# Performance work log

Hardware: AMD Instinct MI355X
Metric: run time of the kernel (lower is better)

Reference implementation:

```python
import jax, jax.numpy as jnp
import numpy as np

N_EMBD = 2048
N_HEAD = 16
N_KV_HEAD = 4
HD = N_EMBD // N_HEAD  # 128
B, T = 1, 4096
EPS = 1e-6


def apply_rope(x, cos, sin):
    # x: [B,T,H,hd]; cos/sin: [T,1,hd//2]
    hd = x.shape[-1] // 2
    x1, x2 = x[..., :hd], x[..., hd:]
    y1 = x1 * cos + x2 * sin
    y2 = x2 * cos - x1 * sin
    return jnp.concatenate((y1, y2), axis=-1).astype(x.dtype)


def rms_norm(x, eps=EPS):
    return x * jax.lax.rsqrt(jnp.mean(jnp.square(x), axis=-1, keepdims=True) + eps)


def setup_inputs() -> dict:
    key = jax.random.key(0)
    ks = jax.random.split(key, 7)
    s = 0.02
    return {
        "x": jax.random.normal(ks[0], (B, T, N_EMBD), dtype=jnp.float32),
        "cos": jax.random.normal(ks[1], (T, 1, HD // 2), dtype=jnp.float32),
        "sin": jax.random.normal(ks[2], (T, 1, HD // 2), dtype=jnp.float32),
        "wq": jax.random.normal(ks[3], (N_EMBD, N_HEAD * HD), dtype=jnp.float32) * s,
        "wk": jax.random.normal(ks[4], (N_EMBD, N_KV_HEAD * HD), dtype=jnp.float32) * s,
        "wv": jax.random.normal(ks[5], (N_EMBD, N_KV_HEAD * HD), dtype=jnp.float32) * s,
        "wo": jax.random.normal(ks[6], (N_EMBD, N_EMBD), dtype=jnp.float32) * s,
    }


def reference(x, cos, sin, wq, wk, wv, wo):
    Bb, Tt, C = x.shape
    q = (x @ wq).reshape(Bb, Tt, N_HEAD, HD)
    k = (x @ wk).reshape(Bb, Tt, N_KV_HEAD, HD)
    v = (x @ wv).reshape(Bb, Tt, N_KV_HEAD, HD)
    q = rms_norm(apply_rope(q, cos, sin))
    k = rms_norm(apply_rope(k, cos, sin))
    g = N_HEAD // N_KV_HEAD
    if g > 1:
        k = jnp.repeat(k, g, axis=2)  # [B,T,H,hd]
        v = jnp.repeat(v, g, axis=2)
    scale = 1.0 / jnp.sqrt(jnp.float32(HD))
    # scores: [B,H,T,S]
    scores = jnp.einsum("bthd,bshd->bhts", q, k) * scale
    causal = jnp.tril(jnp.ones((Tt, Tt), dtype=bool))
    scores = jnp.where(causal, scores, jnp.finfo(scores.dtype).min)
    attn = jax.nn.softmax(scores, axis=-1)
    y = jnp.einsum("bhts,bshd->bthd", attn, v).reshape(Bb, Tt, C)
    return y @ wo
```

## Files before the change

kernel.cpp:

```cpp
#include <hip/hip_runtime.h>

#define T_SEQ 4096
#define C_EMB 2048
#define NH 16
#define NKV 4
#define HD 128

typedef short bf16x8 __attribute__((ext_vector_type(8)));
typedef float f32x4 __attribute__((ext_vector_type(4)));
typedef unsigned short u16x4 __attribute__((ext_vector_type(4)));

__device__ inline unsigned short f2bf(float f) {
    unsigned int u = __float_as_uint(f);
    unsigned int r = (u + 0x7FFFu + ((u >> 16) & 1u)) >> 16;
    return (unsigned short)r;
}

__device__ __forceinline__ void async_cp16(const unsigned short* g, unsigned short* l) {
    __builtin_amdgcn_global_load_lds((const __attribute__((address_space(1))) unsigned int*)g,
                                     (__attribute__((address_space(3))) unsigned int*)l,
                                     16, 0, 0);
}

__global__ __launch_bounds__(256) void cvt_bf16(const float* __restrict__ in,
                                                unsigned short* __restrict__ out, int n) {
    int i = (blockIdx.x * 256 + threadIdx.x) * 4;
    if (i >= n) return;
    float4 f = *(const float4*)(&in[i]);
    u16x4 o;
    o.x = f2bf(f.x); o.y = f2bf(f.y); o.z = f2bf(f.z); o.w = f2bf(f.w);
    *(u16x4*)(&out[i]) = o;
}

__global__ __launch_bounds__(256) void transpose_cvt(const float* __restrict__ in, int ld_in,
                                                     int R, int Cc,
                                                     unsigned short* __restrict__ out, int ld_out) {
    __shared__ float tile[32][33];
    int x = blockIdx.x * 32 + threadIdx.x;
    for (int i = threadIdx.y; i < 32; i += 8) {
        int y = blockIdx.y * 32 + i;
        tile[i][threadIdx.x] = in[(size_t)y * ld_in + x];
    }
    __syncthreads();
    int xo = blockIdx.y * 32 + threadIdx.x;
    for (int i = threadIdx.y; i < 32; i += 8) {
        int yo = blockIdx.x * 32 + i;
        out[(size_t)yo * ld_out + xo] = f2bf(tile[threadIdx.x][i]);
    }
}

__global__ __launch_bounds__(256) void gemm_bt(const unsigned short* __restrict__ A,
                                               const unsigned short* __restrict__ Bt,
                                               float* __restrict__ C, int M, int N, int K) {
    __shared__ __align__(16) unsigned short As[128 * 64];
    __shared__ __align__(16) unsigned short Bs[128 * 64];
    int t = threadIdx.x;
    int w = t >> 6, lane = t & 63;
    int ln = lane & 15, q = lane >> 4;
    int wm = (w >> 1) * 64, wn = (w & 1) * 64;
    int m0 = blockIdx.y * 128, n0 = blockIdx.x * 128;

    f32x4 acc[4][4] = {};

    for (int k0 = 0; k0 < K; k0 += 64) {
        __syncthreads();
#pragma unroll
        for (int s = 0; s < 4; ++s) {
            int L = s * 256 + t;
            int r = L >> 3;
            int c = (L & 7) ^ (r & 7);
            async_cp16(&A[(size_t)(m0 + r) * K + k0 + c * 8], &As[s * 2048 + w * 512]);
            async_cp16(&Bt[(size_t)(n0 + r) * K + k0 + c * 8], &Bs[s * 2048 + w * 512]);
        }
        __syncthreads();
#pragma unroll
        for (int ks = 0; ks < 2; ++ks) {
            int cs = ((ks * 4 + q) ^ (ln & 7)) * 8;
            bf16x8 af[4], bfr[4];
#pragma unroll
            for (int i = 0; i < 4; ++i) af[i] = *(const bf16x8*)(&As[(wm + i * 16 + ln) * 64 + cs]);
#pragma unroll
            for (int j = 0; j < 4; ++j) bfr[j] = *(const bf16x8*)(&Bs[(wn + j * 16 + ln) * 64 + cs]);
#pragma unroll
            for (int i = 0; i < 4; ++i)
#pragma unroll
                for (int j = 0; j < 4; ++j)
                    acc[i][j] = __builtin_amdgcn_mfma_f32_16x16x32_bf16(af[i], bfr[j], acc[i][j], 0, 0, 0);
        }
    }
#pragma unroll
    for (int i = 0; i < 4; ++i)
#pragma unroll
        for (int j = 0; j < 4; ++j)
#pragma unroll
            for (int r = 0; r < 4; ++r) {
                int row = m0 + wm + i * 16 + q * 4 + r;
                int col = n0 + wn + j * 16 + ln;
                C[(size_t)row * N + col] = acc[i][j][r];
            }
}

__global__ __launch_bounds__(256) void rope_rms(const float* __restrict__ QKV,
                                                const float* __restrict__ cosb,
                                                const float* __restrict__ sinb,
                                                unsigned short* __restrict__ Qn,
                                                unsigned short* __restrict__ Kn) {
    int gw = blockIdx.x * 4 + (threadIdx.x >> 6);
    int lane = threadIdx.x & 63;
    int t = gw / 20;
    int h = gw % 20;
    const float* v = QKV + (size_t)t * 3072 + h * 128;
    float a = v[lane];
    float b = v[lane + 64];
    float cc = cosb[t * 64 + lane];
    float ss = sinb[t * 64 + lane];
    float y1 = a * cc + b * ss;
    float y2 = b * cc - a * ss;
    float sq = y1 * y1 + y2 * y2;
#pragma unroll
    for (int off = 1; off < 64; off <<= 1) sq += __shfl_xor(sq, off);
    float r = rsqrtf(sq * (1.0f / 128.0f) + 1e-6f);
    if (h < 16) {
        float s = r * (0.08838834764831845f * 1.4426950408889634f);
        unsigned short* o = Qn + (size_t)t * 2048 + h * 128;
        o[lane] = f2bf(y1 * s);
        o[lane + 64] = f2bf(y2 * s);
    } else {
        unsigned short* o = Kn + (size_t)t * 512 + (h - 16) * 128;
        o[lane] = f2bf(y1 * r);
        o[lane + 64] = f2bf(y2 * r);
    }
}

__global__ __launch_bounds__(256) void flash_attn(const unsigned short* __restrict__ Qn,
                                                  const unsigned short* __restrict__ Kn,
                                                  const unsigned short* __restrict__ Vt,
                                                  unsigned short* __restrict__ Ao) {
    __shared__ __align__(16) unsigned short Ks[2][64 * 128];
    __shared__ __align__(16) unsigned short Vs[2][128 * 64];
    __shared__ __align__(16) unsigned short Pl[4][16 * 72];

    int pairi = blockIdx.x;
    int h = blockIdx.y;
    int kvh = h >> 2;
    int t = threadIdx.x;
    int w = t >> 6, lane = t & 63;
    int ln = lane & 15, q = lane >> 4;

    int nA = 64 - pairi;
    int bq = 63 - pairi;
    int wq0 = bq * 64 + w * 16;

    bf16x8 qf[4];
    {
        const unsigned short* qb = Qn + (size_t)(wq0 + ln) * 2048 + h * 128;
#pragma unroll
        for (int kc = 0; kc < 4; ++kc) qf[kc] = *(const bf16x8*)(qb + kc * 32 + q * 8);
    }

    f32x4 o[8] = {};
    f32x4 l_p = {0.f, 0.f, 0.f, 0.f};

#pragma unroll
    for (int s = 0; s < 4; ++s) {
        int L = s * 256 + t;
        int key = L >> 4;
        int c = (L & 15) ^ (key & 15);
        async_cp16(Kn + (size_t)key * 512 + kvh * 128 + c * 8, &Ks[0][s * 2048 + w * 512]);
    }
#pragma unroll
    for (int s = 0; s < 4; ++s) {
        int L = s * 256 + t;
        int hd = L >> 3;
        int c = (L & 7) ^ (hd & 7);
        async_cp16(Vt + (size_t)(kvh * 128 + hd) * 4096 + c * 8, &Vs[0][s * 2048 + w * 512]);
    }

    for (int it = 0; it < 65; ++it) {
        __syncthreads();

        int nxt = it + 1;
        if (nxt < 65) {
            int nkt = (nxt < nA) ? nxt * 64 : (nxt - nA) * 64;
            unsigned short* kd = Ks[nxt & 1];
            unsigned short* vd = Vs[nxt & 1];
#pragma unroll
            for (int s = 0; s < 4; ++s) {
                int L = s * 256 + t;
                int key = L >> 4;
                int c = (L & 15) ^ (key & 15);
                async_cp16(Kn + (size_t)(nkt + key) * 512 + kvh * 128 + c * 8,
                           kd + s * 2048 + w * 512);
            }
#pragma unroll
            for (int s = 0; s < 4; ++s) {
                int L = s * 256 + t;
                int hd = L >> 3;
                int c = (L & 7) ^ (hd & 7);
                async_cp16(Vt + (size_t)(kvh * 128 + hd) * 4096 + nkt + c * 8,
                           vd + s * 2048 + w * 512);
            }
        }

        if (it == nA) {
#pragma unroll
            for (int r = 0; r < 4; ++r) {
                float lsum = l_p[r];
                lsum += __shfl_xor(lsum, 1);
                lsum += __shfl_xor(lsum, 2);
                lsum += __shfl_xor(lsum, 4);
                lsum += __shfl_xor(lsum, 8);
                float inv = 1.0f / lsum;
                int row = wq0 + q * 4 + r;
                unsigned short* ob = Ao + (size_t)row * 2048 + h * 128;
#pragma unroll
                for (int f = 0; f < 8; ++f) ob[f * 16 + ln] = f2bf(o[f][r] * inv);
            }
            bq = pairi;
            wq0 = bq * 64 + w * 16;
            const unsigned short* qb = Qn + (size_t)(wq0 + ln) * 2048 + h * 128;
#pragma unroll
            for (int kc = 0; kc < 4; ++kc) qf[kc] = *(const bf16x8*)(qb + kc * 32 + q * 8);
#pragma unroll
            for (int f = 0; f < 8; ++f) o[f] = (f32x4){0.f, 0.f, 0.f, 0.f};
            l_p = (f32x4){0.f, 0.f, 0.f, 0.f};
        }

        int kt0 = (it < nA) ? it * 64 : (it - nA) * 64;
        const unsigned short* kb = Ks[it & 1];
        const unsigned short* vb = Vs[it & 1];

        f32x4 sA[4] = {{-16.6f, -16.6f, -16.6f, -16.6f}, {-16.6f, -16.6f, -16.6f, -16.6f},
                       {-16.6f, -16.6f, -16.6f, -16.6f}, {-16.6f, -16.6f, -16.6f, -16.6f}};
#pragma unroll
        for (int jt = 0; jt < 4; ++jt) {
            int key = jt * 16 + ln;
#pragma unroll
            for (int kc = 0; kc < 4; ++kc) {
                int cs = ((kc * 4 + q) ^ ln) * 8;
                bf16x8 kf = *(const bf16x8*)(&kb[key * 128 + cs]);
                sA[jt] = __builtin_amdgcn_mfma_f32_16x16x32_bf16(qf[kc], kf, sA[jt], 0, 0, 0);
            }
        }
        if (kt0 + 63 > wq0) {
#pragma unroll
            for (int jt = 0; jt < 4; ++jt)
#pragma unroll
                for (int r = 0; r < 4; ++r) {
                    int key = kt0 + jt * 16 + ln;
                    int row = wq0 + q * 4 + r;
                    if (key > row) sA[jt][r] = -3e38f;
                }
        }
#pragma unroll
        for (int r = 0; r < 4; ++r) {
            int prow = (q * 4 + r) * 72;
#pragma unroll
            for (int jt = 0; jt < 4; ++jt) {
                float p = __builtin_amdgcn_exp2f(sA[jt][r]);
                Pl[w][prow + jt * 16 + ln] = (unsigned short)(__float_as_uint(p) >> 16);
                l_p[r] += p;
            }
        }

#pragma unroll
        for (int ks = 0; ks < 2; ++ks) {
            bf16x8 pa = *(const bf16x8*)(&Pl[w][ln * 72 + ks * 32 + q * 8]);
            int cs = ((ks * 4 + q) ^ (ln & 7)) * 8;
#pragma unroll
            for (int f = 0; f < 8; ++f) {
                bf16x8 vf = *(const bf16x8*)(&vb[(f * 16 + ln) * 64 + cs]);
                o[f] = __builtin_amdgcn_mfma_f32_16x16x32_bf16(pa, vf, o[f], 0, 0, 0);
            }
        }
    }
#pragma unroll
    for (int r = 0; r < 4; ++r) {
        float lsum = l_p[r];
        lsum += __shfl_xor(lsum, 1);
        lsum += __shfl_xor(lsum, 2);
        lsum += __shfl_xor(lsum, 4);
        lsum += __shfl_xor(lsum, 8);
        float inv = 1.0f / lsum;
        int row = wq0 + q * 4 + r;
        unsigned short* ob = Ao + (size_t)row * 2048 + h * 128;
#pragma unroll
        for (int f = 0; f < 8; ++f) ob[f * 16 + ln] = f2bf(o[f][r] * inv);
    }
}

extern "C" void kernel_launch(void* const* d_in, const int* in_sizes, int n_in,
                              void* d_out, int out_size, void* d_ws, size_t ws_size,
                              hipStream_t stream) {
    const float* x    = (const float*)d_in[0];
    const float* cosb = (const float*)d_in[1];
    const float* sinb = (const float*)d_in[2];
    const float* wq   = (const float*)d_in[3];
    const float* wk   = (const float*)d_in[4];
    const float* wv   = (const float*)d_in[5];
    const float* wo   = (const float*)d_in[6];
    float* out = (float*)d_out;

    char* ws = (char*)d_ws;
    float* QKV = (float*)ws;
    unsigned short* xb    = (unsigned short*)(ws + (size_t)4096 * 3072 * 4);
    unsigned short* wqkvT = xb    + (size_t)4096 * 2048;
    unsigned short* woT   = wqkvT + (size_t)3072 * 2048;
    unsigned short* Qn    = woT   + (size_t)2048 * 2048;
    unsigned short* Kn    = Qn    + (size_t)4096 * 2048;
    unsigned short* Vt    = Kn    + (size_t)4096 * 512;
    unsigned short* Ao    = Vt    + (size_t)512 * 4096;

    cvt_bf16<<<(4096 * 2048 / 4 + 255) / 256, 256, 0, stream>>>(x, xb, 4096 * 2048);
    transpose_cvt<<<dim3(64, 64), dim3(32, 8), 0, stream>>>(wq, 2048, 2048, 2048, wqkvT, 2048);
    transpose_cvt<<<dim3(16, 64), dim3(32, 8), 0, stream>>>(wk, 512, 2048, 512, wqkvT + (size_t)2048 * 2048, 2048);
    transpose_cvt<<<dim3(16, 64), dim3(32, 8), 0, stream>>>(wv, 512, 2048, 512, wqkvT + (size_t)2560 * 2048, 2048);
    transpose_cvt<<<dim3(64, 64), dim3(32, 8), 0, stream>>>(wo, 2048, 2048, 2048, woT, 2048);
    gemm_bt<<<dim3(24, 32), 256, 0, stream>>>(xb, wqkvT, QKV, 4096, 3072, 2048);
    transpose_cvt<<<dim3(16, 128), dim3(32, 8), 0, stream>>>(QKV + 2560, 3072, 4096, 512, Vt, 4096);
    rope_rms<<<4096 * 20 / 4, 256, 0, stream>>>(QKV, cosb, sinb, Qn, Kn);
    flash_attn<<<dim3(32, 16), 256, 0, stream>>>(Qn, Kn, Vt, Ao);
    gemm_bt<<<dim3(16, 32), 256, 0, stream>>>(Ao, woT, out, 4096, 2048, 2048);
}
```

Baseline: 391.5 us.

## Fuse RoPE+RMSNorm into QKV GEMM epilogue and double-buffer GEMM LDS loads

```diff
diff --git a/kernel.cpp b/kernel.cpp
--- a/kernel.cpp
+++ b/kernel.cpp
@@ -49,11 +49,125 @@
     }
 }
 
-__global__ __launch_bounds__(256) void gemm_bt(const unsigned short* __restrict__ A,
-                                               const unsigned short* __restrict__ Bt,
-                                               float* __restrict__ C, int M, int N, int K) {
-    __shared__ __align__(16) unsigned short As[128 * 64];
-    __shared__ __align__(16) unsigned short Bs[128 * 64];
+__global__ __launch_bounds__(256) void gemm_qkv(const unsigned short* __restrict__ A,
+                                                const unsigned short* __restrict__ Bt,
+                                                const float* __restrict__ cosb,
+                                                const float* __restrict__ sinb,
+                                                unsigned short* __restrict__ Qn,
+                                                unsigned short* __restrict__ Kn,
+                                                float* __restrict__ Vbuf) {
+    __shared__ __align__(16) unsigned short As[2][128 * 64];
+    __shared__ __align__(16) unsigned short Bs[2][128 * 64];
+    const int K = 2048;
+    int t = threadIdx.x;
+    int w = t >> 6, lane = t & 63;
+    int ln = lane & 15, q = lane >> 4;
+    int wm = w * 32;
+    int m0 = blockIdx.y * 128, n0 = blockIdx.x * 128;
+
+    f32x4 acc[2][8] = {};
+
+#pragma unroll
+    for (int s = 0; s < 4; ++s) {
+        int L = s * 256 + t;
+        int r = L >> 3;
+        int c = (L & 7) ^ (r & 7);
+        async_cp16(&A[(size_t)(m0 + r) * K + c * 8], &As[0][s * 2048 + w * 512]);
+        async_cp16(&Bt[(size_t)(n0 + r) * K + c * 8], &Bs[0][s * 2048 + w * 512]);
+    }
+
+    for (int it = 0; it < 32; ++it) {
+        __syncthreads();
+        if (it < 31) {
+            int k0 = (it + 1) * 64;
+            int p = (it + 1) & 1;
+#pragma unroll
+            for (int s = 0; s < 4; ++s) {
+                int L = s * 256 + t;
+                int r = L >> 3;
+                int c = (L & 7) ^ (r & 7);
+                async_cp16(&A[(size_t)(m0 + r) * K + k0 + c * 8], &As[p][s * 2048 + w * 512]);
+                async_cp16(&Bt[(size_t)(n0 + r) * K + k0 + c * 8], &Bs[p][s * 2048 + w * 512]);
+            }
+        }
+        int p = it & 1;
+#pragma unroll
+        for (int ks = 0; ks < 2; ++ks) {
+            int cs = ((ks * 4 + q) ^ (ln & 7)) * 8;
+            bf16x8 af[2], bfr[8];
+#pragma unroll
+            for (int i = 0; i < 2; ++i) af[i] = *(const bf16x8*)(&As[p][(wm + i * 16 + ln) * 64 + cs]);
+#pragma unroll
+            for (int j = 0; j < 8; ++j) bfr[j] = *(const bf16x8*)(&Bs[p][(j * 16 + ln) * 64 + cs]);
+#pragma unroll
+            for (int i = 0; i < 2; ++i)
+#pragma unroll
+                for (int j = 0; j < 8; ++j)
+                    acc[i][j] = __builtin_amdgcn_mfma_f32_16x16x32_bf16(af[i], bfr[j], acc[i][j], 0, 0, 0);
+        }
+    }
+
+    if (n0 < 2560) {
+        bool isQ = (n0 < 2048);
+        int h = isQ ? (n0 >> 7) : ((n0 - 2048) >> 7);
+#pragma unroll
+        for (int i = 0; i < 2; ++i)
+#pragma unroll
+            for (int r = 0; r < 4; ++r) {
+                int row = m0 + wm + i * 16 + q * 4 + r;
+                float y1[4], y2[4];
+                float ss = 0.0f;
+#pragma unroll
+                for (int j = 0; j < 4; ++j) {
+                    float a = acc[i][j][r];
+                    float b = acc[i][j + 4][r];
+                    float cc = cosb[row * 64 + j * 16 + ln];
+                    float sv = sinb[row * 64 + j * 16 + ln];
+                    y1[j] = a * cc + b * sv;
+                    y2[j] = b * cc - a * sv;
+                    ss += y1[j] * y1[j] + y2[j] * y2[j];
+                }
+                ss += __shfl_xor(ss, 1);
+                ss += __shfl_xor(ss, 2);
+                ss += __shfl_xor(ss, 4);
+                ss += __shfl_xor(ss, 8);
+                float rv = rsqrtf(ss * (1.0f / 128.0f) + 1e-6f);
+                if (isQ) {
+                    float s = rv * (0.08838834764831845f * 1.4426950408889634f);
+                    unsigned short* ob = Qn + (size_t)row * 2048 + h * 128;
+#pragma unroll
+                    for (int j = 0; j < 4; ++j) {
+                        ob[j * 16 + ln] = f2bf(y1[j] * s);
+                        ob[64 + j * 16 + ln] = f2bf(y2[j] * s);
+                    }
+                } else {
+                    unsigned short* ob = Kn + (size_t)row * 512 + h * 128;
+#pragma unroll
+                    for (int j = 0; j < 4; ++j) {
+                        ob[j * 16 + ln] = f2bf(y1[j] * rv);
+                        ob[64 + j * 16 + ln] = f2bf(y2[j] * rv);
+                    }
+                }
+            }
+    } else {
+        int v0 = n0 - 2560;
+#pragma unroll
+        for (int i = 0; i < 2; ++i)
+#pragma unroll
+            for (int j = 0; j < 8; ++j)
+#pragma unroll
+                for (int r = 0; r < 4; ++r) {
+                    int row = m0 + wm + i * 16 + q * 4 + r;
+                    Vbuf[(size_t)row * 512 + v0 + j * 16 + ln] = acc[i][j][r];
+                }
+    }
+}
+
+__global__ __launch_bounds__(256) void gemm_bt_db(const unsigned short* __restrict__ A,
+                                                  const unsigned short* __restrict__ Bt,
+                                                  float* __restrict__ C, int M, int N, int K) {
+    __shared__ __align__(16) unsigned short As[2][128 * 64];
+    __shared__ __align__(16) unsigned short Bs[2][128 * 64];
     int t = threadIdx.x;
     int w = t >> 6, lane = t & 63;
     int ln = lane & 15, q = lane >> 4;
@@ -62,25 +176,39 @@
 
     f32x4 acc[4][4] = {};
 
-    for (int k0 = 0; k0 < K; k0 += 64) {
+#pragma unroll
+    for (int s = 0; s < 4; ++s) {
+        int L = s * 256 + t;
+        int r = L >> 3;
+        int c = (L & 7) ^ (r & 7);
+        async_cp16(&A[(size_t)(m0 + r) * K + c * 8], &As[0][s * 2048 + w * 512]);
+        async_cp16(&Bt[(size_t)(n0 + r) * K + c * 8], &Bs[0][s * 2048 + w * 512]);
+    }
+
+    int niter = K >> 6;
+    for (int it = 0; it < niter; ++it) {
         __syncthreads();
-#pragma unroll
-        for (int s = 0; s < 4; ++s) {
-            int L = s * 256 + t;
-            int r = L >> 3;
-            int c = (L & 7) ^ (r & 7);
-            async_cp16(&A[(size_t)(m0 + r) * K + k0 + c * 8], &As[s * 2048 + w * 512]);
-            async_cp16(&Bt[(size_t)(n0 + r) * K + k0 + c * 8], &Bs[s * 2048 + w * 512]);
-        }
-        __syncthreads();
+        if (it < niter - 1) {
+            int k0 = (it + 1) * 64;
+            int p = (it + 1) & 1;
+#pragma unroll
+            for (int s = 0; s < 4; ++s) {
+                int L = s * 256 + t;
+                int r = L >> 3;
+                int c = (L & 7) ^ (r & 7);
+                async_cp16(&A[(size_t)(m0 + r) * K + k0 + c * 8], &As[p][s * 2048 + w * 512]);
+                async_cp16(&Bt[(size_t)(n0 + r) * K + k0 + c * 8], &Bs[p][s * 2048 + w * 512]);
+            }
+        }
+        int p = it & 1;
 #pragma unroll
         for (int ks = 0; ks < 2; ++ks) {
             int cs = ((ks * 4 + q) ^ (ln & 7)) * 8;
             bf16x8 af[4], bfr[4];
 #pragma unroll
-            for (int i = 0; i < 4; ++i) af[i] = *(const bf16x8*)(&As[(wm + i * 16 + ln) * 64 + cs]);
-#pragma unroll
-            for (int j = 0; j < 4; ++j) bfr[j] = *(const bf16x8*)(&Bs[(wn + j * 16 + ln) * 64 + cs]);
+            for (int i = 0; i < 4; ++i) af[i] = *(const bf16x8*)(&As[p][(wm + i * 16 + ln) * 64 + cs]);
+#pragma unroll
+            for (int j = 0; j < 4; ++j) bfr[j] = *(const bf16x8*)(&Bs[p][(wn + j * 16 + ln) * 64 + cs]);
 #pragma unroll
             for (int i = 0; i < 4; ++i)
 #pragma unroll
@@ -98,38 +226,6 @@
                 int col = n0 + wn + j * 16 + ln;
                 C[(size_t)row * N + col] = acc[i][j][r];
             }
-}
-
-__global__ __launch_bounds__(256) void rope_rms(const float* __restrict__ QKV,
-                                                const float* __restrict__ cosb,
-                                                const float* __restrict__ sinb,
-                                                unsigned short* __restrict__ Qn,
-                                                unsigned short* __restrict__ Kn) {
-    int gw = blockIdx.x * 4 + (threadIdx.x >> 6);
-    int lane = threadIdx.x & 63;
-    int t = gw / 20;
-    int h = gw % 20;
-    const float* v = QKV + (size_t)t * 3072 + h * 128;
-    float a = v[lane];
-    float b = v[lane + 64];
-    float cc = cosb[t * 64 + lane];
-    float ss = sinb[t * 64 + lane];
-    float y1 = a * cc + b * ss;
-    float y2 = b * cc - a * ss;
-    float sq = y1 * y1 + y2 * y2;
-#pragma unroll
-    for (int off = 1; off < 64; off <<= 1) sq += __shfl_xor(sq, off);
-    float r = rsqrtf(sq * (1.0f / 128.0f) + 1e-6f);
-    if (h < 16) {
-        float s = r * (0.08838834764831845f * 1.4426950408889634f);
-        unsigned short* o = Qn + (size_t)t * 2048 + h * 128;
-        o[lane] = f2bf(y1 * s);
-        o[lane + 64] = f2bf(y2 * s);
-    } else {
-        unsigned short* o = Kn + (size_t)t * 512 + (h - 16) * 128;
-        o[lane] = f2bf(y1 * r);
-        o[lane + 64] = f2bf(y2 * r);
-    }
 }
 
 __global__ __launch_bounds__(256) void flash_attn(const unsigned short* __restrict__ Qn,
@@ -302,7 +398,7 @@
     float* out = (float*)d_out;
 
     char* ws = (char*)d_ws;
-    float* QKV = (float*)ws;
+    float* Vbuf = (float*)ws;
     unsigned short* xb    = (unsigned short*)(ws + (size_t)4096 * 3072 * 4);
     unsigned short* wqkvT = xb    + (size_t)4096 * 2048;
     unsigned short* woT   = wqkvT + (size_t)3072 * 2048;
@@ -316,9 +412,8 @@
     transpose_cvt<<<dim3(16, 64), dim3(32, 8), 0, stream>>>(wk, 512, 2048, 512, wqkvT + (size_t)2048 * 2048, 2048);
     transpose_cvt<<<dim3(16, 64), dim3(32, 8), 0, stream>>>(wv, 512, 2048, 512, wqkvT + (size_t)2560 * 2048, 2048);
     transpose_cvt<<<dim3(64, 64), dim3(32, 8), 0, stream>>>(wo, 2048, 2048, 2048, woT, 2048);
-    gemm_bt<<<dim3(24, 32), 256, 0, stream>>>(xb, wqkvT, QKV, 4096, 3072, 2048);
-    transpose_cvt<<<dim3(16, 128), dim3(32, 8), 0, stream>>>(QKV + 2560, 3072, 4096, 512, Vt, 4096);
-    rope_rms<<<4096 * 20 / 4, 256, 0, stream>>>(QKV, cosb, sinb, Qn, Kn);
+    gemm_qkv<<<dim3(24, 32), 256, 0, stream>>>(xb, wqkvT, cosb, sinb, Qn, Kn, Vbuf);
+    transpose_cvt<<<dim3(16, 128), dim3(32, 8), 0, stream>>>(Vbuf, 512, 4096, 512, Vt, 4096);
     flash_attn<<<dim3(32, 16), 256, 0, stream>>>(Qn, Kn, Vt, Ao);
-    gemm_bt<<<dim3(16, 32), 256, 0, stream>>>(Ao, woT, out, 4096, 2048, 2048);
-}
+    gemm_bt_db<<<dim3(16, 32), 256, 0, stream>>>(Ao, woT, out, 4096, 2048, 2048);
+}
```

Measured after the change: 373.0 us. -4.7%, faster.
